# Kernel optimization log

Hardware: AMD Instinct MI355X
Metric: run time of the kernel (lower is better)

Reference implementation:

```python
import jax, jax.numpy as jnp
import numpy as np

N_NODES = 50000
N_EDGES = 800000
IN_DIM = 128
HID_DIM = 128
OUT_DIM = 128


def setup_inputs() -> dict:
    key = jax.random.key(0)
    k = jax.random.split(key, 8)
    x = jax.random.normal(k[0], (N_NODES, IN_DIM), dtype=jnp.float32)
    edge_index = jax.random.randint(k[1], (2, N_EDGES), 0, N_NODES, dtype=jnp.int64)
    edge_weight = jax.random.uniform(k[2], (N_EDGES,), dtype=jnp.float32)
    # GCNConv params: weight [in, out] (glorot-ish), bias [out]
    W1 = jax.random.normal(k[3], (IN_DIM, HID_DIM), dtype=jnp.float32) / np.sqrt(IN_DIM)
    b1 = jnp.zeros((HID_DIM,), dtype=jnp.float32)
    W2 = jax.random.normal(k[4], (HID_DIM, OUT_DIM), dtype=jnp.float32) / np.sqrt(HID_DIM)
    b2 = jnp.zeros((OUT_DIM,), dtype=jnp.float32)
    return {"x": x, "edge_index": edge_index, "edge_weight": edge_weight,
            "W1": W1, "b1": b1, "W2": W2, "b2": b2}


def gcn_conv(x, W, b, src, dst, ew, n_nodes):
    """PyG GCNConv: add self-loops (weight 1), symmetric D^-1/2 (A+I) D^-1/2 norm."""
    h = x @ W  # [N, out]
    deg = jax.ops.segment_sum(ew, dst, num_segments=n_nodes) + 1.0  # +1 for self loop
    dis = jnp.where(deg > 0, jax.lax.rsqrt(deg), 0.0)  # deg^{-1/2}
    norm = dis[src] * ew * dis[dst]  # [E]
    msg = h[src] * norm[:, None]  # gather + weight -> [E, out]
    agg = jax.ops.segment_sum(msg, dst, num_segments=n_nodes)
    # self-loop contribution: norm_ii = dis[i] * 1 * dis[i]
    agg = agg + h * (dis * dis)[:, None]
    return agg + b


def reference(x, edge_index, edge_weight, W1, b1, W2, b2):
    src, dst = edge_index[0], edge_index[1]
    n = x.shape[0]
    h = gcn_conv(x, W1, b1, src, dst, edge_weight, n)
    h = jax.nn.relu(h)
    out = gcn_conv(h, W2, b2, src, dst, edge_weight, n)
    return out
```

## Files before the change

### kernel.cpp

```cpp
#include <hip/hip_runtime.h>

#define NDIM 128

typedef __attribute__((ext_vector_type(8))) short bf16x8;
typedef __attribute__((ext_vector_type(4))) float floatx4;

__device__ __forceinline__ float bflo(unsigned v){ return __uint_as_float(v << 16); }
__device__ __forceinline__ float bfhi(unsigned v){ return __uint_as_float(v & 0xffff0000u); }
__device__ __forceinline__ unsigned f2bf(float f){
  unsigned u = __float_as_uint(f);
  return (u + 0x7fffu + ((u >> 16) & 1u)) >> 16;
}

__global__ void k_init(unsigned long long* pk, int n){
  int i = blockIdx.x * blockDim.x + threadIdx.x;
  if (i < n) pk[i] = 0ULL;
}

__global__ void k_deg(const int* __restrict__ ei, const float* __restrict__ ew,
                      unsigned long long* pk, int E){
  int e = blockIdx.x * blockDim.x + threadIdx.x;
  if (e >= E) return;
  int d = ei[E + e];
  unsigned fx = (unsigned)__float2uint_rn(ew[e] * 1048576.0f);
  atomicAdd(&pk[d], (1ULL << 44) | (unsigned long long)fx);
}

__global__ __launch_bounds__(1024) void k_scan1(const unsigned long long* __restrict__ pk,
                                                int* __restrict__ off,
                                                int* __restrict__ bsum, int n){
  __shared__ int wsum[16];
  int t = threadIdx.x;
  int i = blockIdx.x * 1024 + t;
  int c = (i < n) ? (int)(pk[i] >> 44) : 0;
  int lane = t & 63, w = t >> 6;
  int v = c;
  #pragma unroll
  for (int d = 1; d < 64; d <<= 1){ int u = __shfl_up(v, d); if (lane >= d) v += u; }
  if (lane == 63) wsum[w] = v;
  __syncthreads();
  if (w == 0){
    int sv = (lane < 16) ? wsum[lane] : 0;
    #pragma unroll
    for (int d = 1; d < 16; d <<= 1){ int u = __shfl_up(sv, d); if (lane >= d) sv += u; }
    if (lane < 16) wsum[lane] = sv;
  }
  __syncthreads();
  int base = (w > 0) ? wsum[w - 1] : 0;
  if (i < n) off[i] = base + v - c;
  if (t == 1023) bsum[blockIdx.x] = wsum[15];
}

__global__ void k_scan2(int* bsum, int nb){
  int lane = threadIdx.x & 63;
  int c = (lane < nb) ? bsum[lane] : 0;
  int v = c;
  #pragma unroll
  for (int d = 1; d < 64; d <<= 1){ int u = __shfl_up(v, d); if (lane >= d) v += u; }
  if (lane < nb) bsum[lane] = v - c;
}

__global__ __launch_bounds__(1024) void k_scan3(int* __restrict__ off, int* __restrict__ cur,
                                                const int* __restrict__ bsum,
                                                const unsigned long long* __restrict__ pk,
                                                float* __restrict__ dis, int n, int E){
  int i = blockIdx.x * 1024 + threadIdx.x;
  if (i == 0) off[n] = E;
  if (i >= n) return;
  int o = off[i] + bsum[blockIdx.x];
  off[i] = o; cur[i] = o;
  float deg = 1.0f + (float)(pk[i] & ((1ULL << 44) - 1)) * (1.0f / 1048576.0f);
  dis[i] = rsqrtf(deg);
}

__global__ void k_place(const int* __restrict__ ei, const float* __restrict__ ew,
                        const float* __restrict__ dis, int* cur, unsigned* edges, int E){
  int e = blockIdx.x * blockDim.x + threadIdx.x;
  if (e >= E) return;
  int s = ei[e], d = ei[E + e];
  int p = atomicAdd(&cur[d], 1);
  edges[p] = (f2bf(dis[s] * ew[e] * dis[d]) << 16) | (unsigned)s;
}

__global__ void k_wprep(const float* __restrict__ W, unsigned short* __restrict__ Wp){
  int t = blockIdx.x * 256 + threadIdx.x;
  int k = t >> 7, n = t & 127;
  int kt = k >> 5, kq = (k >> 3) & 3, j = k & 7;
  int Lb = kq * 16 + (n & 15);
  Wp[(((kt * 8 + (n >> 4)) * 64) + Lb) * 8 + j] = (unsigned short)f2bf(W[t]);
}

template<int XF32>
__global__ __launch_bounds__(256) void k_gemm_mfma(const void* __restrict__ Xv,
                                                   const unsigned short* __restrict__ Wp,
                                                   unsigned short* __restrict__ Hout,
                                                   int ntiles){
  __shared__ unsigned short Wb[4 * 8 * 64 * 8];
  int tid = threadIdx.x;
  for (int t = tid; t < 2048; t += 256)
    ((uint4*)Wb)[t] = ((const uint4*)Wp)[t];
  __syncthreads();

  int w = tid >> 6, L = tid & 63;
  int m = L & 15, q = L >> 4;
  for (int tile = blockIdx.x * 4 + w; tile < ntiles; tile += gridDim.x * 4){
    size_t row = (size_t)tile * 16 + m;
    floatx4 acc[8] = {};
    #pragma unroll
    for (int kt = 0; kt < 4; ++kt){
      bf16x8 a;
      if (XF32){
        const float* xp = (const float*)Xv + row * NDIM + kt * 32 + q * 8;
        float4 a0 = *(const float4*)xp;
        float4 a1 = *(const float4*)(xp + 4);
        unsigned short* as = (unsigned short*)&a;
        as[0] = f2bf(a0.x); as[1] = f2bf(a0.y); as[2] = f2bf(a0.z); as[3] = f2bf(a0.w);
        as[4] = f2bf(a1.x); as[5] = f2bf(a1.y); as[6] = f2bf(a1.z); as[7] = f2bf(a1.w);
      } else {
        a = *(const bf16x8*)((const unsigned short*)Xv + row * NDIM + kt * 32 + q * 8);
      }
      #pragma unroll
      for (int ct = 0; ct < 8; ++ct){
        bf16x8 b = *(const bf16x8*)&Wb[((kt * 8 + ct) * 64 + L) * 8];
        acc[ct] = __builtin_amdgcn_mfma_f32_16x16x32_bf16(a, b, acc[ct], 0, 0, 0);
      }
    }
    #pragma unroll
    for (int ct = 0; ct < 8; ++ct){
      #pragma unroll
      for (int r = 0; r < 4; ++r){
        size_t orow = (size_t)tile * 16 + q * 4 + r;
        Hout[orow * NDIM + ct * 16 + m] = (unsigned short)f2bf(acc[ct][r]);
      }
    }
  }
}

template<int OUT_F32>
__global__ __launch_bounds__(256) void k_agg(const unsigned short* __restrict__ H,
                                             const int* __restrict__ off,
                                             const unsigned* __restrict__ edges,
                                             const float* __restrict__ dis,
                                             const float* __restrict__ bias,
                                             void* __restrict__ out,
                                             int n, int do_relu){
  int g = threadIdx.x >> 6, L = threadIdx.x & 63;
  int i = blockIdx.x * 4 + g;
  if (i >= n) return;
  float di = dis[i];
  float2 bv = ((const float2*)bias)[L];
  unsigned hv = ((const unsigned*)(H + (size_t)i * NDIM))[L];
  float acc0 = bv.x + bflo(hv) * di * di;
  float acc1 = bv.y + bfhi(hv) * di * di;
  int p = off[i], p1 = off[i + 1];
  while (p + 8 <= p1){
    unsigned e[8], h[8];
    #pragma unroll
    for (int j = 0; j < 8; ++j) e[j] = edges[p + j];
    #pragma unroll
    for (int j = 0; j < 8; ++j)
      h[j] = ((const unsigned*)(H + (size_t)(e[j] & 0xFFFF) * NDIM))[L];
    #pragma unroll
    for (int j = 0; j < 8; ++j){
      float w = bfhi(e[j]);
      acc0 = fmaf(bflo(h[j]), w, acc0);
      acc1 = fmaf(bfhi(h[j]), w, acc1);
    }
    p += 8;
  }
  for (; p < p1; ++p){
    unsigned e = edges[p];
    unsigned h2 = ((const unsigned*)(H + (size_t)(e & 0xFFFF) * NDIM))[L];
    float w = bfhi(e);
    acc0 = fmaf(bflo(h2), w, acc0);
    acc1 = fmaf(bfhi(h2), w, acc1);
  }
  if (do_relu){ acc0 = fmaxf(acc0, 0.f); acc1 = fmaxf(acc1, 0.f); }
  if (OUT_F32){
    ((float2*)((float*)out + (size_t)i * NDIM))[L] = make_float2(acc0, acc1);
  } else {
    ((unsigned*)((unsigned short*)out + (size_t)i * NDIM))[L] = (f2bf(acc1) << 16) | f2bf(acc0);
  }
}

extern "C" void kernel_launch(void* const* d_in, const int* in_sizes, int n_in,
                              void* d_out, int out_size, void* d_ws, size_t ws_size,
                              hipStream_t stream){
  const float* x  = (const float*)d_in[0];
  const int*   ei = (const int*)  d_in[1];
  const float* ew = (const float*)d_in[2];
  const float* W1 = (const float*)d_in[3];
  const float* b1 = (const float*)d_in[4];
  const float* W2 = (const float*)d_in[5];
  const float* b2 = (const float*)d_in[6];
  float* out = (float*)d_out;
  int N = in_sizes[0] / NDIM;
  int E = in_sizes[2];
  int nb = (N + 1023) / 1024;
  int ntiles = N / 16;

  char* p = (char*)d_ws;
  auto alloc = [&](size_t b) -> char* { char* r = p; p += (b + 255) & ~(size_t)255; return r; };
  unsigned long long* pk = (unsigned long long*)alloc((size_t)N * 8);
  float*    dis   = (float*)   alloc((size_t)N * 4);
  int*      cur   = (int*)     alloc((size_t)N * 4);
  int*      off   = (int*)     alloc((size_t)(N + 1) * 4);
  int*      bsum  = (int*)     alloc((size_t)64 * 4);
  unsigned short* Wp1 = (unsigned short*)alloc(NDIM * NDIM * 2);
  unsigned short* Wp2 = (unsigned short*)alloc(NDIM * NDIM * 2);
  unsigned* edges = (unsigned*)alloc((size_t)E * 4);
  unsigned short* R = (unsigned short*)alloc((size_t)N * NDIM * 2);
  unsigned short* H1 = (unsigned short*)d_out;

  k_init <<<(N + 255) / 256, 256, 0, stream>>>(pk, N);
  k_deg  <<<(E + 255) / 256, 256, 0, stream>>>(ei, ew, pk, E);
  k_scan1<<<nb, 1024, 0, stream>>>(pk, off, bsum, N);
  k_scan2<<<1, 64, 0, stream>>>(bsum, nb);
  k_scan3<<<nb, 1024, 0, stream>>>(off, cur, bsum, pk, dis, N, E);
  k_place<<<(E + 255) / 256, 256, 0, stream>>>(ei, ew, dis, cur, edges, E);
  k_wprep<<<64, 256, 0, stream>>>(W1, Wp1);
  k_wprep<<<64, 256, 0, stream>>>(W2, Wp2);

  k_gemm_mfma<1><<<512, 256, 0, stream>>>(x, Wp1, H1, ntiles);
  k_agg<0> <<<(N + 3) / 4, 256, 0, stream>>>(H1, off, edges, dis, b1, R, N, 1);
  k_gemm_mfma<0><<<512, 256, 0, stream>>>(R, Wp2, R, ntiles);
  k_agg<1> <<<(N + 3) / 4, 256, 0, stream>>>(R, off, edges, dis, b2, out, N, 0);
}
```

Baseline: 265.9 us.

## Fuse CSR preprocessing kernels into one cooperative kernel with grid syncs

Replaces the eight small preprocessing launches (init, degree, three scan passes, place, two weight preps) with one cooperative kernel that separates phases with grid-wide syncs. Each thread also caches its first few edge records in registers so the placement pass does not reload them. The GEMM grid is resized to one wave per 16-row tile instead of a fixed 512 blocks. This removes launch gaps and repeated edge reads, but adds grid-sync cost and assumes 256 blocks of 1024 threads can be co-resident.

```diff
diff --git a/kernel.cpp b/kernel.cpp
--- a/kernel.cpp
+++ b/kernel.cpp
@@ -1,6 +1,12 @@
 #include <hip/hip_runtime.h>
+#include <hip/hip_cooperative_groups.h>
+
+namespace cg = cooperative_groups;
 
 #define NDIM 128
+#define PRE_GRID 256
+#define PRE_BLK 1024
+#define NSLOT 4
 
 typedef __attribute__((ext_vector_type(8))) short bf16x8;
 typedef __attribute__((ext_vector_type(4))) float floatx4;
@@ -12,82 +18,96 @@
   return (u + 0x7fffu + ((u >> 16) & 1u)) >> 16;
 }
 
-__global__ void k_init(unsigned long long* pk, int n){
-  int i = blockIdx.x * blockDim.x + threadIdx.x;
-  if (i < n) pk[i] = 0ULL;
-}
-
-__global__ void k_deg(const int* __restrict__ ei, const float* __restrict__ ew,
-                      unsigned long long* pk, int E){
-  int e = blockIdx.x * blockDim.x + threadIdx.x;
-  if (e >= E) return;
-  int d = ei[E + e];
-  unsigned fx = (unsigned)__float2uint_rn(ew[e] * 1048576.0f);
-  atomicAdd(&pk[d], (1ULL << 44) | (unsigned long long)fx);
-}
-
-__global__ __launch_bounds__(1024) void k_scan1(const unsigned long long* __restrict__ pk,
-                                                int* __restrict__ off,
-                                                int* __restrict__ bsum, int n){
+__global__ __launch_bounds__(PRE_BLK, 4) void k_pre(
+    const int* __restrict__ ei, const float* __restrict__ ew,
+    const float* __restrict__ W1, const float* __restrict__ W2,
+    unsigned long long* __restrict__ pk, int* __restrict__ off,
+    int* __restrict__ cur, int* __restrict__ bsum, float* __restrict__ dis,
+    unsigned* __restrict__ edges, unsigned short* __restrict__ Wp1,
+    unsigned short* __restrict__ Wp2, int N, int E, int nb)
+{
+  cg::grid_group grid = cg::this_grid();
   __shared__ int wsum[16];
+  __shared__ int sBase;
   int t = threadIdx.x;
-  int i = blockIdx.x * 1024 + t;
-  int c = (i < n) ? (int)(pk[i] >> 44) : 0;
-  int lane = t & 63, w = t >> 6;
-  int v = c;
-  #pragma unroll
-  for (int d = 1; d < 64; d <<= 1){ int u = __shfl_up(v, d); if (lane >= d) v += u; }
-  if (lane == 63) wsum[w] = v;
-  __syncthreads();
-  if (w == 0){
-    int sv = (lane < 16) ? wsum[lane] : 0;
-    #pragma unroll
-    for (int d = 1; d < 16; d <<= 1){ int u = __shfl_up(sv, d); if (lane >= d) sv += u; }
-    if (lane < 16) wsum[lane] = sv;
-  }
-  __syncthreads();
-  int base = (w > 0) ? wsum[w - 1] : 0;
-  if (i < n) off[i] = base + v - c;
-  if (t == 1023) bsum[blockIdx.x] = wsum[15];
-}
-
-__global__ void k_scan2(int* bsum, int nb){
-  int lane = threadIdx.x & 63;
-  int c = (lane < nb) ? bsum[lane] : 0;
-  int v = c;
-  #pragma unroll
-  for (int d = 1; d < 64; d <<= 1){ int u = __shfl_up(v, d); if (lane >= d) v += u; }
-  if (lane < nb) bsum[lane] = v - c;
-}
-
-__global__ __launch_bounds__(1024) void k_scan3(int* __restrict__ off, int* __restrict__ cur,
-                                                const int* __restrict__ bsum,
-                                                const unsigned long long* __restrict__ pk,
-                                                float* __restrict__ dis, int n, int E){
-  int i = blockIdx.x * 1024 + threadIdx.x;
-  if (i == 0) off[n] = E;
-  if (i >= n) return;
-  int o = off[i] + bsum[blockIdx.x];
-  off[i] = o; cur[i] = o;
-  float deg = 1.0f + (float)(pk[i] & ((1ULL << 44) - 1)) * (1.0f / 1048576.0f);
-  dis[i] = rsqrtf(deg);
-}
-
-__global__ void k_place(const int* __restrict__ ei, const float* __restrict__ ew,
-                        const float* __restrict__ dis, int* cur, unsigned* edges, int E){
-  int e = blockIdx.x * blockDim.x + threadIdx.x;
-  if (e >= E) return;
-  int s = ei[e], d = ei[E + e];
-  int p = atomicAdd(&cur[d], 1);
-  edges[p] = (f2bf(dis[s] * ew[e] * dis[d]) << 16) | (unsigned)s;
-}
-
-__global__ void k_wprep(const float* __restrict__ W, unsigned short* __restrict__ Wp){
-  int t = blockIdx.x * 256 + threadIdx.x;
-  int k = t >> 7, n = t & 127;
-  int kt = k >> 5, kq = (k >> 3) & 3, j = k & 7;
-  int Lb = kq * 16 + (n & 15);
-  Wp[(((kt * 8 + (n >> 4)) * 64) + Lb) * 8 + j] = (unsigned short)f2bf(W[t]);
+  int gtid = blockIdx.x * PRE_BLK + t;
+  int gstride = PRE_GRID * PRE_BLK;
+
+  for (int i = gtid; i < N; i += gstride) pk[i] = 0ULL;
+  for (int tt = gtid; tt < NDIM * NDIM; tt += gstride){
+    int k = tt >> 7, n = tt & 127;
+    int kt = k >> 5, kq = (k >> 3) & 3, j = k & 7;
+    int Lb = kq * 16 + (n & 15);
+    int idx = (((kt * 8 + (n >> 4)) * 64) + Lb) * 8 + j;
+    Wp1[idx] = (unsigned short)f2bf(W1[tt]);
+    Wp2[idx] = (unsigned short)f2bf(W2[tt]);
+  }
+  grid.sync();
+
+  int es[NSLOT], ed[NSLOT];
+  float ewr[NSLOT];
+  int ne = 0;
+  for (int e = gtid; e < E; e += gstride){
+    int s = ei[e], d = ei[E + e];
+    float w = ew[e];
+    if (ne < NSLOT){ es[ne] = s; ed[ne] = d; ewr[ne] = w; }
+    ++ne;
+    unsigned fx = (unsigned)__float2uint_rn(w * 1048576.0f);
+    atomicAdd(&pk[d], (1ULL << 44) | (unsigned long long)fx);
+  }
+  grid.sync();
+
+  if (blockIdx.x < (unsigned)nb){
+    int i = blockIdx.x * 1024 + t;
+    int c = (i < N) ? (int)(pk[i] >> 44) : 0;
+    int lane = t & 63, w = t >> 6;
+    int v = c;
+    #pragma unroll
+    for (int d = 1; d < 64; d <<= 1){ int u = __shfl_up(v, d); if (lane >= d) v += u; }
+    if (lane == 63) wsum[w] = v;
+    __syncthreads();
+    if (w == 0){
+      int sv = (lane < 16) ? wsum[lane] : 0;
+      #pragma unroll
+      for (int d = 1; d < 16; d <<= 1){ int u = __shfl_up(sv, d); if (lane >= d) sv += u; }
+      if (lane < 16) wsum[lane] = sv;
+    }
+    __syncthreads();
+    int base = (w > 0) ? wsum[w - 1] : 0;
+    if (i < N) off[i] = base + v - c;
+    if (t == 1023) bsum[blockIdx.x] = wsum[15];
+  }
+  grid.sync();
+
+  if (blockIdx.x < (unsigned)nb){
+    if (t < 64){
+      int c2 = (t < nb) ? bsum[t] : 0;
+      int v2 = c2;
+      #pragma unroll
+      for (int d = 1; d < 64; d <<= 1){ int u = __shfl_up(v2, d); if (t >= d) v2 += u; }
+      if (t == (int)blockIdx.x) sBase = v2 - c2;
+    }
+    __syncthreads();
+    int i = blockIdx.x * 1024 + t;
+    if (i == 0) off[N] = E;
+    if (i < N){
+      int o = off[i] + sBase;
+      off[i] = o; cur[i] = o;
+      float deg = 1.0f + (float)(pk[i] & ((1ULL << 44) - 1)) * (1.0f / 1048576.0f);
+      dis[i] = rsqrtf(deg);
+    }
+  }
+  grid.sync();
+
+  int cnt = 0;
+  for (int e = gtid; e < E; e += gstride){
+    int s, d; float w;
+    if (cnt < NSLOT){ s = es[cnt]; d = ed[cnt]; w = ewr[cnt]; }
+    else { s = ei[e]; d = ei[E + e]; w = ew[e]; }
+    ++cnt;
+    int p = atomicAdd(&cur[d], 1);
+    edges[p] = (f2bf(dis[s] * w * dis[d]) << 16) | (unsigned)s;
+  }
 }
 
 template<int XF32>
@@ -212,17 +232,18 @@
   unsigned short* R = (unsigned short*)alloc((size_t)N * NDIM * 2);
   unsigned short* H1 = (unsigned short*)d_out;
 
-  k_init <<<(N + 255) / 256, 256, 0, stream>>>(pk, N);
-  k_deg  <<<(E + 255) / 256, 256, 0, stream>>>(ei, ew, pk, E);
-  k_scan1<<<nb, 1024, 0, stream>>>(pk, off, bsum, N);
-  k_scan2<<<1, 64, 0, stream>>>(bsum, nb);
-  k_scan3<<<nb, 1024, 0, stream>>>(off, cur, bsum, pk, dis, N, E);
-  k_place<<<(E + 255) / 256, 256, 0, stream>>>(ei, ew, dis, cur, edges, E);
-  k_wprep<<<64, 256, 0, stream>>>(W1, Wp1);
-  k_wprep<<<64, 256, 0, stream>>>(W2, Wp2);
-
-  k_gemm_mfma<1><<<512, 256, 0, stream>>>(x, Wp1, H1, ntiles);
+  {
+    void* args[] = { (void*)&ei, (void*)&ew, (void*)&W1, (void*)&W2,
+                     (void*)&pk, (void*)&off, (void*)&cur, (void*)&bsum,
+                     (void*)&dis, (void*)&edges, (void*)&Wp1, (void*)&Wp2,
+                     (void*)&N, (void*)&E, (void*)&nb };
+    hipLaunchCooperativeKernel((const void*)k_pre, dim3(PRE_GRID), dim3(PRE_BLK),
+                               args, 0, stream);
+  }
+
+  int gg = (ntiles + 3) / 4;
+  k_gemm_mfma<1><<<gg, 256, 0, stream>>>(x, Wp1, H1, ntiles);
   k_agg<0> <<<(N + 3) / 4, 256, 0, stream>>>(H1, off, edges, dis, b1, R, N, 1);
-  k_gemm_mfma<0><<<512, 256, 0, stream>>>(R, Wp2, R, ntiles);
+  k_gemm_mfma<0><<<gg, 256, 0, stream>>>(R, Wp2, R, ntiles);
   k_agg<1> <<<(N + 3) / 4, 256, 0, stream>>>(R, off, edges, dis, b2, out, N, 0);
 }
```

Measured after the change: 394.9 us. 48.6% more time.
